# Kernel optimization log

Measured on AMD Instinct MI355X. Metric: run time of the kernel, lower is better.

Reference implementation:

```python
import jax, jax.numpy as jnp
import numpy as np

B, T, D, H, L, V = 2, 1024, 1024, 4, 4, 32000  # H redefined below
H = 16            # n_heads
HD = D // H       # head_size = 64
NL = 4            # n_layer
EPS = 1e-5


def _layernorm(x, scale, bias):
    mu = jnp.mean(x, axis=-1, keepdims=True)
    var = jnp.mean(jnp.square(x - mu), axis=-1, keepdims=True)
    return (x - mu) * jax.lax.rsqrt(var + EPS) * scale + bias


def setup_inputs() -> dict:
    key = jax.random.key(0)
    ks = iter(jax.random.split(key, 40))
    s = lambda shape: jax.random.normal(next(ks), shape, jnp.float32) * 0.02
    inp = {
        'idx': jax.random.randint(next(ks), (B, T), 0, V),
        'tok_emb': s((V, D)),
        'pos_emb': s((T, D)),
        # per-layer stacked params (leading axis = layer)
        'Wq': s((NL, D, D)), 'Wk': s((NL, D, D)), 'Wv': s((NL, D, D)),
        'Wo': s((NL, D, D)), 'bo': jnp.zeros((NL, D), jnp.float32),
        'ln1_s': jnp.ones((NL, D), jnp.float32), 'ln1_b': jnp.zeros((NL, D), jnp.float32),
        'ln2_s': jnp.ones((NL, D), jnp.float32), 'ln2_b': jnp.zeros((NL, D), jnp.float32),
        'W1': s((NL, D, 4 * D)), 'b1': jnp.zeros((NL, 4 * D), jnp.float32),
        'W2': s((NL, 4 * D, D)), 'b2': jnp.zeros((NL, D), jnp.float32),
        'lnf_s': jnp.ones((D,), jnp.float32), 'lnf_b': jnp.zeros((D,), jnp.float32),
        'Wlm': s((D, V)), 'blm': jnp.zeros((V,), jnp.float32),
    }
    return inp


def reference(idx, tok_emb, pos_emb, Wq, Wk, Wv, Wo, bo,
              ln1_s, ln1_b, ln2_s, ln2_b, W1, b1, W2, b2,
              lnf_s, lnf_b, Wlm, blm):
    b, t = idx.shape
    x = tok_emb[idx] + pos_emb[None, :t]            # [B,T,D]
    causal = jnp.tril(jnp.ones((t, t), bool))        # [T,T]
    scale = 1.0 / np.sqrt(HD).astype(np.float32)
    for l in range(NL):
        h = _layernorm(x, ln1_s[l], ln1_b[l])
        q = (h @ Wq[l]).reshape(b, t, H, HD)
        k = (h @ Wk[l]).reshape(b, t, H, HD)
        v = (h @ Wv[l]).reshape(b, t, H, HD)
        scores = jnp.einsum('bthd,bshd->bhts', q, k) * scale
        scores = jnp.where(causal[None, None], scores, -jnp.inf)
        attn = jax.nn.softmax(scores, axis=-1)       # [B,H,T,T]
        o = jnp.einsum('bhts,bshd->bthd', attn, v).reshape(b, t, D)
        x = x + o @ Wo[l] + bo[l]
        h2 = _layernorm(x, ln2_s[l], ln2_b[l])
        x = x + jax.nn.relu(h2 @ W1[l] + b1[l]) @ W2[l] + b2[l]
    x = _layernorm(x, lnf_s, lnf_b)
    logits = x @ Wlm + blm                           # [B,T,V]
    return logits
```

## Files before the change

### kernel.cpp

```cpp
#include <hip/hip_runtime.h>

typedef unsigned short u16;
typedef unsigned int u32;
typedef __bf16 bf16x8 __attribute__((ext_vector_type(8)));
typedef float f32x4 __attribute__((ext_vector_type(4)));
typedef u16 u16x8 __attribute__((ext_vector_type(8)));
typedef u16 u16x4 __attribute__((ext_vector_type(4)));

static __device__ __forceinline__ u16 f2bf(float f) {
  u32 u = __builtin_bit_cast(u32, f);
  u32 r = (u + 0x7FFFu + ((u >> 16) & 1u)) >> 16;
  return (u16)r;
}

#define GLOAD_LDS16(gp, lp)                                                   \
  __builtin_amdgcn_global_load_lds(                                           \
      (const __attribute__((address_space(1))) void*)(gp),                    \
      (__attribute__((address_space(3))) void*)(lp), 16, 0, 0)

__global__ void k_embed(const int* __restrict__ idx, const float* __restrict__ tok,
                        const float* __restrict__ pos, float* __restrict__ x) {
  int row = blockIdx.x;
  int t = row & 1023;
  int id = idx[row];
  int c = threadIdx.x * 4;
  float4 a = *(const float4*)(tok + (size_t)id * 1024 + c);
  float4 p = *(const float4*)(pos + (size_t)t * 1024 + c);
  float4 r{a.x + p.x, a.y + p.y, a.z + p.z, a.w + p.w};
  *(float4*)(x + (size_t)row * 1024 + c) = r;
}

__global__ void k_ln(const float* __restrict__ x, const float* __restrict__ sc,
                     const float* __restrict__ bi, u16* __restrict__ out) {
  int row = blockIdx.x;
  int t = threadIdx.x;
  const float* xr = x + (size_t)row * 1024;
  float4 v = *(const float4*)(xr + t * 4);
  float s = v.x + v.y + v.z + v.w;
  float ss = v.x * v.x + v.y * v.y + v.z * v.z + v.w * v.w;
  for (int d = 1; d < 64; d <<= 1) { s += __shfl_xor(s, d); ss += __shfl_xor(ss, d); }
  __shared__ float red[8];
  int wave = t >> 6, lane = t & 63;
  if (lane == 0) { red[wave] = s; red[wave + 4] = ss; }
  __syncthreads();
  s = red[0] + red[1] + red[2] + red[3];
  ss = red[4] + red[5] + red[6] + red[7];
  float mu = s * (1.0f / 1024.0f);
  float var = ss * (1.0f / 1024.0f) - mu * mu;
  float inv = rsqrtf(var + 1e-5f);
  float4 g = *(const float4*)(sc + t * 4);
  float4 b = *(const float4*)(bi + t * 4);
  u16x4 o;
  o[0] = f2bf((v.x - mu) * inv * g.x + b.x);
  o[1] = f2bf((v.y - mu) * inv * g.y + b.y);
  o[2] = f2bf((v.z - mu) * inv * g.z + b.z);
  o[3] = f2bf((v.w - mu) * inv * g.w + b.w);
  *(u16x4*)(out + (size_t)row * 1024 + t * 4) = o;
}

__launch_bounds__(1024)
__global__ void k_transpose(const float* __restrict__ src, u16* __restrict__ dst,
                            int R, int C) {
  __shared__ float tile[32][33];
  int tx = threadIdx.x, ty = threadIdx.y;
  int c = blockIdx.x * 32 + tx;
  int r = blockIdx.y * 32 + ty;
  tile[ty][tx] = src[(size_t)r * C + c];
  __syncthreads();
  int dr = blockIdx.x * 32 + ty;
  int dc = blockIdx.y * 32 + tx;
  dst[(size_t)dr * R + dc] = f2bf(tile[tx][ty]);
}

__launch_bounds__(1024)
__global__ void k_transpose_layer(const float* __restrict__ Wq, const float* __restrict__ Wk,
                                  const float* __restrict__ Wv, const float* __restrict__ Wo,
                                  const float* __restrict__ W1, const float* __restrict__ W2,
                                  u16* __restrict__ qkvT, u16* __restrict__ WoT,
                                  u16* __restrict__ W1T, u16* __restrict__ W2T) {
  int bid = blockIdx.x;
  const float* src; u16* dst; int R, C, bx, by;
  if (bid < 4096) {
    int which = bid >> 10, tile_i = bid & 1023;
    bx = tile_i & 31; by = tile_i >> 5; R = 1024; C = 1024;
    src = which == 0 ? Wq : which == 1 ? Wk : which == 2 ? Wv : Wo;
    dst = which == 3 ? WoT : qkvT + (size_t)which * 1048576;
  } else if (bid < 8192) {
    int tile_i = bid - 4096; bx = tile_i & 127; by = tile_i >> 7; R = 1024; C = 4096;
    src = W1; dst = W1T;
  } else {
    int tile_i = bid - 8192; bx = tile_i & 31; by = tile_i >> 5; R = 4096; C = 1024;
    src = W2; dst = W2T;
  }
  __shared__ float tile[32][33];
  int tx = threadIdx.x, ty = threadIdx.y;
  int c = bx * 32 + tx, r = by * 32 + ty;
  tile[ty][tx] = src[(size_t)r * C + c];
  __syncthreads();
  int dr = bx * 32 + ty, dc = by * 32 + tx;
  dst[(size_t)dr * R + dc] = f2bf(tile[tx][ty]);
}

enum { EPI_QKV = 0, EPI_RELU = 2 };

template <int EPI>
__launch_bounds__(256, 4)
__global__ void k_gemm64(const u16* __restrict__ A, const u16* __restrict__ Bt,
                         const float* __restrict__ bias, u16* __restrict__ bout,
                         int M, int N, int K) {
  __shared__ alignas(16) u16 smem[12288];
#define AL(s, r, k) smem[(s)*2048 + (r)*32 + (k)]
#define BL(s, r, k) smem[4096 + (s)*4096 + (r)*32 + (k)]
  const int t = threadIdx.x;
  const int wave = t >> 6, lane = t & 63;
  const int wm = wave >> 1, wn = wave & 1;
  const int g = lane >> 4, c = lane & 15;
  const int m0 = blockIdx.x * 64, n0 = blockIdx.y * 128;

  const int rwA = t >> 2, sgA = (t & 3) * 8;
  const u16* gA = A + (size_t)(m0 + rwA) * K + sgA;
  const u16* gB = Bt + (size_t)(n0 + rwA) * K + sgA;

  f32x4 acc[2][4] = {};
  const int nK = K >> 5;
  int cur = 0;

  GLOAD_LDS16(gA, &AL(0, rwA, 0));
#pragma unroll
  for (int p = 0; p < 2; ++p)
    GLOAD_LDS16(gB + (size_t)p * 64 * K, &BL(0, p * 64 + rwA, 0));
  __syncthreads();

  for (int kt = 0; kt < nK; ++kt) {
    if (kt + 1 < nK) {
      const int k0 = (kt + 1) << 5;
      GLOAD_LDS16(gA + k0, &AL(cur ^ 1, rwA, 0));
#pragma unroll
      for (int p = 0; p < 2; ++p)
        GLOAD_LDS16(gB + k0 + (size_t)p * 64 * K, &BL(cur ^ 1, p * 64 + rwA, 0));
    }
    bf16x8 af[2], bfr[4];
#pragma unroll
    for (int i = 0; i < 2; ++i)
      af[i] = *(const bf16x8*)&AL(cur, wm * 32 + i * 16 + c, g * 8);
#pragma unroll
    for (int j = 0; j < 4; ++j)
      bfr[j] = *(const bf16x8*)&BL(cur, wn * 64 + j * 16 + c, g * 8);
#pragma unroll
    for (int i = 0; i < 2; ++i)
#pragma unroll
      for (int j = 0; j < 4; ++j)
        acc[i][j] = __builtin_amdgcn_mfma_f32_16x16x32_bf16(af[i], bfr[j], acc[i][j], 0, 0, 0);
    __syncthreads();
    cur ^= 1;
  }

  if (EPI == EPI_QKV) {
    const int which = n0 >> 10;
    const int b = m0 >> 10, t0 = m0 & 1023;
    const int hh0 = (n0 >> 6) & 15;
    if (which < 2) {
      u16 (*Ct)[136] = (u16(*)[136])smem;
#pragma unroll
      for (int i = 0; i < 2; ++i)
#pragma unroll
        for (int j = 0; j < 4; ++j)
#pragma unroll
          for (int r = 0; r < 4; ++r)
            Ct[wm * 32 + i * 16 + g * 4 + r][wn * 64 + j * 16 + c] = f2bf(acc[i][j][r]);
      __syncthreads();
      u16* obase = bout + (size_t)which * 2097152;
#pragma unroll
      for (int itr = 0; itr < 4; ++itr) {
        int idx2 = itr * 256 + t;
        int s = idx2 >> 9;
        int tt = (idx2 >> 3) & 63;
        int seg = idx2 & 7;
        u16x8 vv = *(const u16x8*)&Ct[tt][s * 64 + seg * 8];
        *(u16x8*)(obase + ((size_t)(b * 16 + hh0 + s) * 1024 + (t0 + tt)) * 64 + seg * 8) = vv;
      }
    } else {
      u16 (*Cv)[72] = (u16(*)[72])smem;
#pragma unroll
      for (int i = 0; i < 2; ++i)
#pragma unroll
        for (int j = 0; j < 4; ++j) {
          u16x4 pk;
#pragma unroll
          for (int r = 0; r < 4; ++r) pk[r] = f2bf(acc[i][j][r]);
          *(u16x4*)&Cv[wn * 64 + j * 16 + c][wm * 32 + i * 16 + g * 4] = pk;
        }
      __syncthreads();
      u16* obase = bout + (size_t)2 * 2097152;
#pragma unroll
      for (int itr = 0; itr < 4; ++itr) {
        int idx2 = itr * 256 + t;
        int row = idx2 >> 3;
        int seg = idx2 & 7;
        int s = row >> 6, f = row & 63;
        u16x8 vv = *(const u16x8*)&Cv[row][seg * 8];
        *(u16x8*)(obase + ((size_t)(b * 16 + hh0 + s) * 64 + f) * 1024 + t0 + seg * 8) = vv;
      }
    }
  } else {
    u16 (*Ct)[136] = (u16(*)[136])smem;
#pragma unroll
    for (int i = 0; i < 2; ++i)
#pragma unroll
      for (int j = 0; j < 4; ++j)
#pragma unroll
        for (int r = 0; r < 4; ++r) {
          float u = acc[i][j][r] + bias[n0 + wn * 64 + j * 16 + c];
          Ct[wm * 32 + i * 16 + g * 4 + r][wn * 64 + j * 16 + c] = f2bf(u > 0.f ? u : 0.f);
        }
    __syncthreads();
#pragma unroll
    for (int itr = 0; itr < 4; ++itr) {
      int idx2 = itr * 256 + t;
      int tt = idx2 >> 4, seg = idx2 & 15;
      *(u16x8*)(bout + (size_t)(m0 + tt) * N + n0 + seg * 8) =
          *(const u16x8*)&Ct[tt][seg * 8];
    }
  }
#undef AL
#undef BL
}

__launch_bounds__(256, 8)
__global__ void k_gemm_res(const u16* __restrict__ A, const u16* __restrict__ Bt,
                           const float* __restrict__ bias, float* __restrict__ fout,
                           int M, int N, int K) {
  __shared__ alignas(16) u16 smem[8192];
  const int t = threadIdx.x;
  const int wave = t >> 6, lane = t & 63;
  const int wm = wave >> 1, wn = wave & 1;
  const int g = lane >> 4, c = lane & 15;
  const int m0 = blockIdx.x * 64, n0 = blockIdx.y * 64;

  const int rw = t >> 2, sg = (t & 3) * 8;
  const u16* gA = A + (size_t)(m0 + rw) * K + sg;
  const u16* gB = Bt + (size_t)(n0 + rw) * K + sg;

  f32x4 acc[2][2] = {};
  const int nK = K >> 5;
  int cur = 0;

  GLOAD_LDS16(gA, &smem[rw * 32]);
  GLOAD_LDS16(gB, &smem[4096 + rw * 32]);
  __syncthreads();

  for (int kt = 0; kt < nK; ++kt) {
    if (kt + 1 < nK) {
      const int k0 = (kt + 1) << 5;
      GLOAD_LDS16(gA + k0, &smem[(cur ^ 1) * 2048 + rw * 32]);
      GLOAD_LDS16(gB + k0, &smem[4096 + (cur ^ 1) * 2048 + rw * 32]);
    }
    bf16x8 af[2], bfr[2];
#pragma unroll
    for (int i = 0; i < 2; ++i)
      af[i] = *(const bf16x8*)&smem[cur * 2048 + (wm * 32 + i * 16 + c) * 32 + g * 8];
#pragma unroll
    for (int j = 0; j < 2; ++j)
      bfr[j] = *(const bf16x8*)&smem[4096 + cur * 2048 + (wn * 32 + j * 16 + c) * 32 + g * 8];
#pragma unroll
    for (int i = 0; i < 2; ++i)
#pragma unroll
      for (int j = 0; j < 2; ++j)
        acc[i][j] = __builtin_amdgcn_mfma_f32_16x16x32_bf16(af[i], bfr[j], acc[i][j], 0, 0, 0);
    __syncthreads();
    cur ^= 1;
  }

#pragma unroll
  for (int i = 0; i < 2; ++i)
#pragma unroll
    for (int j = 0; j < 2; ++j)
#pragma unroll
      for (int r = 0; r < 4; ++r) {
        int m = m0 + wm * 32 + i * 16 + g * 4 + r;
        int n = n0 + wn * 32 + j * 16 + c;
        fout[(size_t)m * N + n] += acc[i][j][r] + bias[n];
      }
}

__launch_bounds__(256, 4)
__global__ void k_gemm_out(const u16* __restrict__ A, const u16* __restrict__ Bt,
                           const float* __restrict__ bias, float* __restrict__ fout,
                           int M, int N, int K) {
  __shared__ alignas(16) u16 sm[2][2][128][32];
  const int t = threadIdx.x;
  const int wave = t >> 6, lane = t & 63;
  const int wm = wave >> 1, wn = wave & 1;
  const int g = lane >> 4, c = lane & 15;
  const int m0 = blockIdx.x * 128, n0 = blockIdx.y * 128;

  const int srow = wave * 32 + (lane >> 2);
  const int sseg = (lane & 3) * 8;
  const u16* gA = A + (size_t)(m0 + srow) * K + sseg;
  const u16* gB = Bt + (size_t)(n0 + srow) * K + sseg;

  f32x4 acc[4][4] = {};
  const int nK = K >> 5;
  int cur = 0;

#pragma unroll
  for (int p = 0; p < 2; ++p) {
    GLOAD_LDS16(gA + (size_t)p * 16 * K, &sm[0][0][wave * 32 + p * 16][0]);
    GLOAD_LDS16(gB + (size_t)p * 16 * K, &sm[0][1][wave * 32 + p * 16][0]);
  }
  __syncthreads();

  for (int kt = 0; kt < nK; ++kt) {
    if (kt + 1 < nK) {
      const int k0 = (kt + 1) << 5;
#pragma unroll
      for (int p = 0; p < 2; ++p) {
        GLOAD_LDS16(gA + k0 + (size_t)p * 16 * K, &sm[cur ^ 1][0][wave * 32 + p * 16][0]);
        GLOAD_LDS16(gB + k0 + (size_t)p * 16 * K, &sm[cur ^ 1][1][wave * 32 + p * 16][0]);
      }
    }
    bf16x8 af[4], bfr[4];
#pragma unroll
    for (int i = 0; i < 4; ++i) {
      af[i]  = *(const bf16x8*)&sm[cur][0][wm * 64 + i * 16 + c][g * 8];
      bfr[i] = *(const bf16x8*)&sm[cur][1][wn * 64 + i * 16 + c][g * 8];
    }
#pragma unroll
    for (int i = 0; i < 4; ++i)
#pragma unroll
      for (int j = 0; j < 4; ++j)
        acc[i][j] = __builtin_amdgcn_mfma_f32_16x16x32_bf16(af[i], bfr[j], acc[i][j], 0, 0, 0);
    __syncthreads();
    cur ^= 1;
  }

  float (*st)[132] = (float(*)[132])sm;
#pragma unroll
  for (int i = 0; i < 4; ++i) {
#pragma unroll
    for (int j = 0; j < 4; ++j)
#pragma unroll
      for (int r = 0; r < 4; ++r)
        st[wm * 16 + g * 4 + r][wn * 64 + j * 16 + c] = acc[i][j][r];
    __syncthreads();
    {
      int row = t >> 3;
      int cs = (t & 7) * 16;
      int m = m0 + (row >> 4) * 64 + i * 16 + (row & 15);
      float* dst = fout + (size_t)m * N + n0 + cs;
#pragma unroll
      for (int q = 0; q < 4; ++q) {
        float4 v = *(const float4*)&st[row][cs + q * 4];
        float4 bb = *(const float4*)&bias[n0 + cs + q * 4];
        float4 o{v.x + bb.x, v.y + bb.y, v.z + bb.z, v.w + bb.w};
        *(float4*)(dst + q * 4) = o;
      }
    }
    __syncthreads();
  }
}

__launch_bounds__(64)
__global__ void k_attn(const u16* __restrict__ Q, const u16* __restrict__ Kb,
                       const u16* __restrict__ VT, u16* __restrict__ O) {
  const int qb = blockIdx.x;
  const int bh = blockIdx.y;
  const int lane = threadIdx.x;
  const int g = lane >> 4, c = lane & 15;
  const int q0 = qb << 5;
  const u16* Qh = Q + (size_t)bh * 65536;
  const u16* Kh = Kb + (size_t)bh * 65536;
  const u16* VTh = VT + (size_t)bh * 65536;

  __shared__ u16 Pl[32][40];

  bf16x8 aq[2][2];
#pragma unroll
  for (int qt = 0; qt < 2; ++qt) {
    aq[qt][0] = *(const bf16x8*)(Qh + (q0 + qt * 16 + c) * 64 + g * 8);
    aq[qt][1] = *(const bf16x8*)(Qh + (q0 + qt * 16 + c) * 64 + 32 + g * 8);
  }

  f32x4 Oacc[2][4] = {};
  float Mr[2][4], Lr[2][4] = {};
#pragma unroll
  for (int qt = 0; qt < 2; ++qt)
#pragma unroll
    for (int r = 0; r < 4; ++r) Mr[qt][r] = -1e30f;

  const int nIt = qb + 1;
  for (int it = 0; it < nIt; ++it) {
    const int k0 = it << 5;
    bf16x8 b0 = *(const bf16x8*)(Kh + (k0 + c) * 64 + g * 8);
    bf16x8 b1 = *(const bf16x8*)(Kh + (k0 + c) * 64 + 32 + g * 8);
    bf16x8 b2 = *(const bf16x8*)(Kh + (k0 + 16 + c) * 64 + g * 8);
    bf16x8 b3 = *(const bf16x8*)(Kh + (k0 + 16 + c) * 64 + 32 + g * 8);
    f32x4 S[2][2];
#pragma unroll
    for (int qt = 0; qt < 2; ++qt) {
      f32x4 z = {};
      S[qt][0] = __builtin_amdgcn_mfma_f32_16x16x32_bf16(
          aq[qt][1], b1, __builtin_amdgcn_mfma_f32_16x16x32_bf16(aq[qt][0], b0, z, 0, 0, 0), 0, 0, 0);
      S[qt][1] = __builtin_amdgcn_mfma_f32_16x16x32_bf16(
          aq[qt][1], b3, __builtin_amdgcn_mfma_f32_16x16x32_bf16(aq[qt][0], b2, z, 0, 0, 0), 0, 0, 0);
    }
    const float scale = 0.125f;
    float sv[2][2][4], mt[2][4];
    float need = 0.0f;
#pragma unroll
    for (int qt = 0; qt < 2; ++qt)
#pragma unroll
      for (int r = 0; r < 4; ++r) {
        int q = q0 + qt * 16 + (g << 2) + r;
        float s0 = (k0 + c <= q) ? S[qt][0][r] * scale : -1e30f;
        float s1 = (k0 + 16 + c <= q) ? S[qt][1][r] * scale : -1e30f;
        sv[qt][0][r] = s0; sv[qt][1][r] = s1;
        float m = fmaxf(s0, s1);
        m = fmaxf(m, __shfl_xor(m, 1));
        m = fmaxf(m, __shfl_xor(m, 2));
        m = fmaxf(m, __shfl_xor(m, 4));
        m = fmaxf(m, __shfl_xor(m, 8));
        mt[qt][r] = m;
        need = fmaxf(need, m - Mr[qt][r]);
      }
    const bool nore = __all(need <= 8.0f);
#pragma unroll
    for (int qt = 0; qt < 2; ++qt)
#pragma unroll
      for (int r = 0; r < 4; ++r) {
        float mn = nore ? Mr[qt][r] : fmaxf(Mr[qt][r], mt[qt][r]);
        float p0 = __expf(sv[qt][0][r] - mn);
        float p1 = __expf(sv[qt][1][r] - mn);
        float rs = p0 + p1;
        rs += __shfl_xor(rs, 1);
        rs += __shfl_xor(rs, 2);
        rs += __shfl_xor(rs, 4);
        rs += __shfl_xor(rs, 8);
        if (nore) {
          Lr[qt][r] += rs;
        } else {
          float alpha = __expf(Mr[qt][r] - mn);
          Lr[qt][r] = Lr[qt][r] * alpha + rs;
          Mr[qt][r] = mn;
#pragma unroll
          for (int nb = 0; nb < 4; ++nb) Oacc[qt][nb][r] *= alpha;
        }
        Pl[qt * 16 + (g << 2) + r][c] = f2bf(p0);
        Pl[qt * 16 + (g << 2) + r][16 + c] = f2bf(p1);
      }
#pragma unroll
    for (int nb = 0; nb < 4; ++nb) {
      bf16x8 bv = *(const bf16x8*)(VTh + (size_t)(nb * 16 + c) * 1024 + k0 + g * 8);
#pragma unroll
      for (int qt = 0; qt < 2; ++qt) {
        bf16x8 ap = *(const bf16x8*)&Pl[qt * 16 + c][g * 8];
        Oacc[qt][nb] = __builtin_amdgcn_mfma_f32_16x16x32_bf16(ap, bv, Oacc[qt][nb], 0, 0, 0);
      }
    }
  }
  const int b = bh >> 4, hh = bh & 15;
#pragma unroll
  for (int qt = 0; qt < 2; ++qt)
#pragma unroll
    for (int r = 0; r < 4; ++r) {
      int tt = q0 + qt * 16 + (g << 2) + r;
      float invl = 1.0f / Lr[qt][r];
#pragma unroll
      for (int nb = 0; nb < 4; ++nb) {
        int d = nb * 16 + c;
        O[((size_t)(b * 1024 + tt)) * 1024 + hh * 64 + d] = f2bf(Oacc[qt][nb][r] * invl);
      }
    }
}

extern "C" void kernel_launch(void* const* d_in, const int* in_sizes, int n_in,
                              void* d_out, int out_size, void* d_ws, size_t ws_size,
                              hipStream_t stream) {
  const int*   idx  = (const int*)d_in[0];
  const float* tok  = (const float*)d_in[1];
  const float* pos  = (const float*)d_in[2];
  const float* Wq   = (const float*)d_in[3];
  const float* Wk   = (const float*)d_in[4];
  const float* Wv   = (const float*)d_in[5];
  const float* Wo   = (const float*)d_in[6];
  const float* bo   = (const float*)d_in[7];
  const float* ln1s = (const float*)d_in[8];
  const float* ln1b = (const float*)d_in[9];
  const float* ln2s = (const float*)d_in[10];
  const float* ln2b = (const float*)d_in[11];
  const float* W1   = (const float*)d_in[12];
  const float* b1   = (const float*)d_in[13];
  const float* W2   = (const float*)d_in[14];
  const float* b2   = (const float*)d_in[15];
  const float* lnfs = (const float*)d_in[16];
  const float* lnfb = (const float*)d_in[17];
  const float* Wlm  = (const float*)d_in[18];
  const float* blm  = (const float*)d_in[19];
  float* out = (float*)d_out;

  char* w = (char*)d_ws;
  auto alloc = [&](size_t bytes) {
    char* p = w;
    w += (bytes + 255) & ~(size_t)255;
    return p;
  };
  float* x  = (float*)alloc(2048ull * 1024 * 4);
  u16* h    = (u16*)alloc(2048ull * 1024 * 2);
  u16* qkv  = (u16*)alloc(3ull * 2097152 * 2);
  u16* o    = (u16*)alloc(2048ull * 1024 * 2);
  u16* a1   = (u16*)alloc(2048ull * 4096 * 2);
  u16* arena = (u16*)alloc(32000ull * 1024 * 2);

  dim3 b32(32, 32, 1);

  k_embed<<<2048, 256, 0, stream>>>(idx, tok, pos, x);

  for (int l = 0; l < 4; ++l) {
    u16* qkvT = arena;
    u16* WoT  = arena + 3ull * 1048576;
    u16* W1T  = arena + 4ull * 1048576;
    u16* W2T  = arena + 8ull * 1048576;
    k_transpose_layer<<<12288, b32, 0, stream>>>(
        Wq + (size_t)l * 1048576, Wk + (size_t)l * 1048576,
        Wv + (size_t)l * 1048576, Wo + (size_t)l * 1048576,
        W1 + (size_t)l * 4194304, W2 + (size_t)l * 4194304,
        qkvT, WoT, W1T, W2T);

    k_ln<<<2048, 256, 0, stream>>>(x, ln1s + l * 1024, ln1b + l * 1024, h);
    k_gemm64<EPI_QKV><<<dim3(32, 24), 256, 0, stream>>>(h, qkvT, nullptr, qkv,
                                                        2048, 3072, 1024);
    k_attn<<<dim3(32, 32), 64, 0, stream>>>(qkv, qkv + 2097152, qkv + 2 * 2097152, o);
    k_gemm_res<<<dim3(32, 16), 256, 0, stream>>>(o, WoT, bo + l * 1024, x,
                                                 2048, 1024, 1024);
    k_ln<<<2048, 256, 0, stream>>>(x, ln2s + l * 1024, ln2b + l * 1024, h);
    k_gemm64<EPI_RELU><<<dim3(32, 32), 256, 0, stream>>>(h, W1T, b1 + l * 4096, a1,
                                                         2048, 4096, 1024);
    k_gemm_res<<<dim3(32, 16), 256, 0, stream>>>(a1, W2T, b2 + l * 1024, x,
                                                 2048, 1024, 4096);
  }

  k_ln<<<2048, 256, 0, stream>>>(x, lnfs, lnfb, h);
  k_transpose<<<dim3(1000, 32), b32, 0, stream>>>(Wlm, arena, 1024, 32000);
  k_gemm_out<<<dim3(16, 250), 256, 0, stream>>>(h, arena, blm, out, 2048, 32000, 1024);
}
```

Baseline: 1.251 ms.

## Split attention KV across two waves, split-K residual GEMMs with atomics, fuse embed+LN

Attention blocks now use two waves that each process half the causal key range and merge their partial softmax states through shared memory. The residual GEMMs split K in two along a z grid dimension and accumulate into x with fp32 atomics, with bias added only by the first slice. The embedding is fused with the first layer's layernorm, and the LM-head GEMM uses a remapped 1D grid for better cache locality. These changes add parallelism for underfilled kernels, at the cost of atomic traffic, nondeterministic summation, and a per-half-wave rescale vote.

```diff
diff --git a/kernel.cpp b/kernel.cpp
--- a/kernel.cpp
+++ b/kernel.cpp
@@ -13,21 +13,47 @@
   return (u16)r;
 }
 
+static __device__ __forceinline__ void atomAddF32(float* p, float v) {
+  asm volatile("global_atomic_add_f32 %0, %1, off" :: "v"(p), "v"(v) : "memory");
+}
+
 #define GLOAD_LDS16(gp, lp)                                                   \
   __builtin_amdgcn_global_load_lds(                                           \
       (const __attribute__((address_space(1))) void*)(gp),                    \
       (__attribute__((address_space(3))) void*)(lp), 16, 0, 0)
 
-__global__ void k_embed(const int* __restrict__ idx, const float* __restrict__ tok,
-                        const float* __restrict__ pos, float* __restrict__ x) {
+__global__ void k_embed_ln(const int* __restrict__ idx, const float* __restrict__ tok,
+                           const float* __restrict__ pos, const float* __restrict__ sc,
+                           const float* __restrict__ bi, float* __restrict__ x,
+                           u16* __restrict__ out) {
   int row = blockIdx.x;
-  int t = row & 1023;
+  int tt = row & 1023;
   int id = idx[row];
-  int c = threadIdx.x * 4;
-  float4 a = *(const float4*)(tok + (size_t)id * 1024 + c);
-  float4 p = *(const float4*)(pos + (size_t)t * 1024 + c);
-  float4 r{a.x + p.x, a.y + p.y, a.z + p.z, a.w + p.w};
-  *(float4*)(x + (size_t)row * 1024 + c) = r;
+  int t = threadIdx.x;
+  float4 a = *(const float4*)(tok + (size_t)id * 1024 + t * 4);
+  float4 p = *(const float4*)(pos + (size_t)tt * 1024 + t * 4);
+  float4 v{a.x + p.x, a.y + p.y, a.z + p.z, a.w + p.w};
+  *(float4*)(x + (size_t)row * 1024 + t * 4) = v;
+  float s = v.x + v.y + v.z + v.w;
+  float ss = v.x * v.x + v.y * v.y + v.z * v.z + v.w * v.w;
+  for (int d = 1; d < 64; d <<= 1) { s += __shfl_xor(s, d); ss += __shfl_xor(ss, d); }
+  __shared__ float red[8];
+  int wave = t >> 6, lane = t & 63;
+  if (lane == 0) { red[wave] = s; red[wave + 4] = ss; }
+  __syncthreads();
+  s = red[0] + red[1] + red[2] + red[3];
+  ss = red[4] + red[5] + red[6] + red[7];
+  float mu = s * (1.0f / 1024.0f);
+  float var = ss * (1.0f / 1024.0f) - mu * mu;
+  float inv = rsqrtf(var + 1e-5f);
+  float4 g = *(const float4*)(sc + t * 4);
+  float4 b = *(const float4*)(bi + t * 4);
+  u16x4 o;
+  o[0] = f2bf((v.x - mu) * inv * g.x + b.x);
+  o[1] = f2bf((v.y - mu) * inv * g.y + b.y);
+  o[2] = f2bf((v.z - mu) * inv * g.z + b.z);
+  o[3] = f2bf((v.w - mu) * inv * g.w + b.w);
+  *(u16x4*)(out + (size_t)row * 1024 + t * 4) = o;
 }
 
 __global__ void k_ln(const float* __restrict__ x, const float* __restrict__ sc,
@@ -236,13 +262,16 @@
   const int wm = wave >> 1, wn = wave & 1;
   const int g = lane >> 4, c = lane & 15;
   const int m0 = blockIdx.x * 64, n0 = blockIdx.y * 64;
+  const int kz = blockIdx.z;
+  const int Kh = K >> 1;
+  const int kbase = kz * Kh;
 
   const int rw = t >> 2, sg = (t & 3) * 8;
-  const u16* gA = A + (size_t)(m0 + rw) * K + sg;
-  const u16* gB = Bt + (size_t)(n0 + rw) * K + sg;
+  const u16* gA = A + (size_t)(m0 + rw) * K + kbase + sg;
+  const u16* gB = Bt + (size_t)(n0 + rw) * K + kbase + sg;
 
   f32x4 acc[2][2] = {};
-  const int nK = K >> 5;
+  const int nK = Kh >> 5;
   int cur = 0;
 
   GLOAD_LDS16(gA, &smem[rw * 32]);
@@ -279,7 +308,8 @@
       for (int r = 0; r < 4; ++r) {
         int m = m0 + wm * 32 + i * 16 + g * 4 + r;
         int n = n0 + wn * 32 + j * 16 + c;
-        fout[(size_t)m * N + n] += acc[i][j][r] + bias[n];
+        float v = acc[i][j][r] + (kz == 0 ? bias[n] : 0.f);
+        atomAddF32(&fout[(size_t)m * N + n], v);
       }
 }
 
@@ -292,7 +322,8 @@
   const int wave = t >> 6, lane = t & 63;
   const int wm = wave >> 1, wn = wave & 1;
   const int g = lane >> 4, c = lane & 15;
-  const int m0 = blockIdx.x * 128, n0 = blockIdx.y * 128;
+  const int wg = (blockIdx.x & 7) * 500 + (blockIdx.x >> 3);
+  const int m0 = (wg & 15) * 128, n0 = (wg >> 4) * 128;
 
   const int srow = wave * 32 + (lane >> 2);
   const int sseg = (lane & 3) * 8;
@@ -360,19 +391,22 @@
   }
 }
 
-__launch_bounds__(64)
+__launch_bounds__(128)
 __global__ void k_attn(const u16* __restrict__ Q, const u16* __restrict__ Kb,
                        const u16* __restrict__ VT, u16* __restrict__ O) {
   const int qb = blockIdx.x;
   const int bh = blockIdx.y;
-  const int lane = threadIdx.x;
+  const int tid = threadIdx.x;
+  const int wv = tid >> 6;
+  const int lane = tid & 63;
   const int g = lane >> 4, c = lane & 15;
   const int q0 = qb << 5;
   const u16* Qh = Q + (size_t)bh * 65536;
   const u16* Kh = Kb + (size_t)bh * 65536;
   const u16* VTh = VT + (size_t)bh * 65536;
 
-  __shared__ u16 Pl[32][40];
+  __shared__ u16 Pl[2][32][40];
+  __shared__ float mrg[64][48];
 
   bf16x8 aq[2][2];
 #pragma unroll
@@ -389,7 +423,11 @@
     for (int r = 0; r < 4; ++r) Mr[qt][r] = -1e30f;
 
   const int nIt = qb + 1;
-  for (int it = 0; it < nIt; ++it) {
+  const int half = (nIt + 1) >> 1;
+  const int itBeg = wv ? half : 0;
+  const int itEnd = wv ? nIt : half;
+
+  for (int it = itBeg; it < itEnd; ++it) {
     const int k0 = it << 5;
     bf16x8 b0 = *(const bf16x8*)(Kh + (k0 + c) * 64 + g * 8);
     bf16x8 b1 = *(const bf16x8*)(Kh + (k0 + c) * 64 + 32 + g * 8);
@@ -423,7 +461,9 @@
         mt[qt][r] = m;
         need = fmaxf(need, m - Mr[qt][r]);
       }
-    const bool nore = __all(need <= 8.0f);
+    unsigned long long vote = __ballot(need <= 8.0f);
+    const bool nore = wv ? ((vote >> 32) == 0xFFFFFFFFull ? true : ((vote & 0xFFFFFFFF00000000ull) == 0xFFFFFFFF00000000ull))
+                         : ((vote & 0xFFFFFFFFull) == 0xFFFFFFFFull);
 #pragma unroll
     for (int qt = 0; qt < 2; ++qt)
 #pragma unroll
@@ -445,32 +485,59 @@
 #pragma unroll
           for (int nb = 0; nb < 4; ++nb) Oacc[qt][nb][r] *= alpha;
         }
-        Pl[qt * 16 + (g << 2) + r][c] = f2bf(p0);
-        Pl[qt * 16 + (g << 2) + r][16 + c] = f2bf(p1);
+        Pl[wv][qt * 16 + (g << 2) + r][c] = f2bf(p0);
+        Pl[wv][qt * 16 + (g << 2) + r][16 + c] = f2bf(p1);
       }
 #pragma unroll
     for (int nb = 0; nb < 4; ++nb) {
       bf16x8 bv = *(const bf16x8*)(VTh + (size_t)(nb * 16 + c) * 1024 + k0 + g * 8);
 #pragma unroll
       for (int qt = 0; qt < 2; ++qt) {
-        bf16x8 ap = *(const bf16x8*)&Pl[qt * 16 + c][g * 8];
+        bf16x8 ap = *(const bf16x8*)&Pl[wv][qt * 16 + c][g * 8];
         Oacc[qt][nb] = __builtin_amdgcn_mfma_f32_16x16x32_bf16(ap, bv, Oacc[qt][nb], 0, 0, 0);
       }
     }
   }
-  const int b = bh >> 4, hh = bh & 15;
-#pragma unroll
-  for (int qt = 0; qt < 2; ++qt)
-#pragma unroll
-    for (int r = 0; r < 4; ++r) {
-      int tt = q0 + qt * 16 + (g << 2) + r;
-      float invl = 1.0f / Lr[qt][r];
-#pragma unroll
-      for (int nb = 0; nb < 4; ++nb) {
-        int d = nb * 16 + c;
-        O[((size_t)(b * 1024 + tt)) * 1024 + hh * 64 + d] = f2bf(Oacc[qt][nb][r] * invl);
-      }
-    }
+
+  if (wv == 1) {
+#pragma unroll
+    for (int qt = 0; qt < 2; ++qt) {
+#pragma unroll
+      for (int nb = 0; nb < 4; ++nb)
+#pragma unroll
+        for (int r = 0; r < 4; ++r)
+          mrg[lane][qt * 16 + nb * 4 + r] = Oacc[qt][nb][r];
+#pragma unroll
+      for (int r = 0; r < 4; ++r) {
+        mrg[lane][32 + qt * 4 + r] = Mr[qt][r];
+        mrg[lane][40 + qt * 4 + r] = Lr[qt][r];
+      }
+    }
+  }
+  __syncthreads();
+  if (wv == 0) {
+    const int b = bh >> 4, hh = bh & 15;
+#pragma unroll
+    for (int qt = 0; qt < 2; ++qt)
+#pragma unroll
+      for (int r = 0; r < 4; ++r) {
+        float m1 = mrg[lane][32 + qt * 4 + r];
+        float l1 = mrg[lane][40 + qt * 4 + r];
+        float mm = fmaxf(Mr[qt][r], m1);
+        float a0 = __expf(Mr[qt][r] - mm);
+        float a1 = __expf(m1 - mm);
+        float l = a0 * Lr[qt][r] + a1 * l1;
+        float invl = 1.0f / l;
+        int tt = q0 + qt * 16 + (g << 2) + r;
+#pragma unroll
+        for (int nb = 0; nb < 4; ++nb) {
+          float o1 = mrg[lane][qt * 16 + nb * 4 + r];
+          float val = (a0 * Oacc[qt][nb][r] + a1 * o1) * invl;
+          int d = nb * 16 + c;
+          O[((size_t)(b * 1024 + tt)) * 1024 + hh * 64 + d] = f2bf(val);
+        }
+      }
+  }
 }
 
 extern "C" void kernel_launch(void* const* d_in, const int* in_sizes, int n_in,
@@ -513,7 +580,7 @@
 
   dim3 b32(32, 32, 1);
 
-  k_embed<<<2048, 256, 0, stream>>>(idx, tok, pos, x);
+  k_embed_ln<<<2048, 256, 0, stream>>>(idx, tok, pos, ln1s, ln1b, x, h);
 
   for (int l = 0; l < 4; ++l) {
     u16* qkvT = arena;
@@ -526,20 +593,21 @@
         W1 + (size_t)l * 4194304, W2 + (size_t)l * 4194304,
         qkvT, WoT, W1T, W2T);
 
-    k_ln<<<2048, 256, 0, stream>>>(x, ln1s + l * 1024, ln1b + l * 1024, h);
+    if (l > 0)
+      k_ln<<<2048, 256, 0, stream>>>(x, ln1s + l * 1024, ln1b + l * 1024, h);
     k_gemm64<EPI_QKV><<<dim3(32, 24), 256, 0, stream>>>(h, qkvT, nullptr, qkv,
                                                         2048, 3072, 1024);
-    k_attn<<<dim3(32, 32), 64, 0, stream>>>(qkv, qkv + 2097152, qkv + 2 * 2097152, o);
-    k_gemm_res<<<dim3(32, 16), 256, 0, stream>>>(o, WoT, bo + l * 1024, x,
-                                                 2048, 1024, 1024);
+    k_attn<<<dim3(32, 32), 128, 0, stream>>>(qkv, qkv + 2097152, qkv + 2 * 2097152, o);
+    k_gemm_res<<<dim3(32, 16, 2), 256, 0, stream>>>(o, WoT, bo + l * 1024, x,
+                                                    2048, 1024, 1024);
     k_ln<<<2048, 256, 0, stream>>>(x, ln2s + l * 1024, ln2b + l * 1024, h);
     k_gemm64<EPI_RELU><<<dim3(32, 32), 256, 0, stream>>>(h, W1T, b1 + l * 4096, a1,
                                                          2048, 4096, 1024);
-    k_gemm_res<<<dim3(32, 16), 256, 0, stream>>>(a1, W2T, b2 + l * 1024, x,
-                                                 2048, 1024, 4096);
+    k_gemm_res<<<dim3(32, 16, 2), 256, 0, stream>>>(a1, W2T, b2 + l * 1024, x,
+                                                    2048, 1024, 4096);
   }
 
   k_ln<<<2048, 256, 0, stream>>>(x, lnfs, lnfb, h);
   k_transpose<<<dim3(1000, 32), b32, 0, stream>>>(Wlm, arena, 1024, 32000);
-  k_gemm_out<<<dim3(16, 250), 256, 0, stream>>>(h, arena, blm, out, 2048, 32000, 1024);
-}
+  k_gemm_out<<<4000, 256, 0, stream>>>(h, arena, blm, out, 2048, 32000, 1024);
+}
```

After: 1.137 ms. -9.1%, faster.
